# Kernel tuning notes

Hardware: AMD Instinct MI355X
Metric: run time of the kernel (lower is better)

Reference implementation:

```python
import jax, jax.numpy as jnp
import numpy as np
from jax import lax

B, L, D, H, DK, DFF, NL = 8, 128, 512, 8, 64, 2048, 6
T = 3 * L - 1
SC, AC = 14, 73  # state / action channel counts


def _linear(x, w, b):
    return x @ w.T + b


def _ln(x, w, b):
    m = x.mean(-1, keepdims=True)
    v = ((x - m) ** 2).mean(-1, keepdims=True)
    return (x - m) / jnp.sqrt(v + 1e-5) * w + b


def _conv(x, w, b):
    y = lax.conv_general_dilated(x, w, (1, 1), ((1, 1), (1, 1)),
                                 dimension_numbers=('NCHW', 'OIHW', 'NCHW'))
    return y + b[None, :, None, None]


def _convT(x, w, b, s, op):
    # torch ConvTranspose2d(k=3, stride=s, padding=1, output_padding=op)
    wt = jnp.flip(w, (2, 3)).transpose(1, 0, 2, 3)
    y = lax.conv_general_dilated(x, wt, (1, 1), ((1, 1 + op), (1, 1 + op)),
                                 lhs_dilation=(s, s),
                                 dimension_numbers=('NCHW', 'OIHW', 'NCHW'))
    return y + b[None, :, None, None]


def _cnn_enc(x, c1w, c1b, c2w, c2b, c3w, c3b, fcw, fcb, lnw, lnb):
    h = jax.nn.relu(_conv(x, c1w, c1b))
    h = jax.nn.relu(_conv(h, c2w, c2b))
    h = jax.nn.relu(_conv(h, c3w, c3b))
    h = h.reshape(h.shape[0], -1)
    return _ln(_linear(h, fcw, fcb), lnw, lnb)


def _mlp_enc(x, w1, b1, w2, b2, lnw, lnb):
    h = jax.nn.relu(_linear(x, w1, b1))
    return _ln(_linear(h, w2, b2), lnw, lnb)


def _decode(z, fcw, fcb, w1, b1, w2, b2, w3, b3):
    h = jax.nn.relu(_linear(z, fcw, fcb)).reshape(-1, 128, 2, 2)
    h = jax.nn.relu(_convT(h, w1, b1, 2, 1))
    h = jax.nn.relu(_convT(h, w2, b2, 2, 1))
    return _convT(h, w3, b3, 1, 0)


def setup_inputs():
    key = jax.random.key(0)
    cnt = [0]
    def nrm(shape, scale=0.02):
        cnt[0] += 1
        return jax.random.normal(jax.random.fold_in(key, cnt[0]), shape, jnp.float32) * scale
    z = lambda *s: jnp.zeros(s, jnp.float32)
    o = lambda *s: jnp.ones(s, jnp.float32)
    inp = dict(
        states=nrm((B, L, SC, 8, 8), 1.0),
        rtgs=nrm((B, L, 1), 1.0),
        timesteps=jax.random.randint(jax.random.fold_in(key, 9999), (B, L, 1), 0, 512, jnp.int32),
        actions=nrm((B, L - 1, AC, 8, 8), 1.0),
        mask=jnp.tril(jnp.ones((T, T), jnp.int32)),
        se_c1w=nrm((32, SC, 3, 3)), se_c1b=z(32),
        se_c2w=nrm((64, 32, 3, 3)), se_c2b=z(64),
        se_c3w=nrm((64, 64, 3, 3)), se_c3b=z(64),
        se_fcw=nrm((D, 64 * 64)), se_fcb=z(D), se_lnw=o(D), se_lnb=z(D),
        ae_c1w=nrm((32, AC, 3, 3)), ae_c1b=z(32),
        ae_c2w=nrm((64, 32, 3, 3)), ae_c2b=z(64),
        ae_c3w=nrm((64, 64, 3, 3)), ae_c3b=z(64),
        ae_fcw=nrm((D, 64 * 64)), ae_fcb=z(D), ae_lnw=o(D), ae_lnb=z(D),
        rtg_w1=nrm((D, 1)), rtg_b1=z(D), rtg_w2=nrm((D, D)), rtg_b2=z(D), rtg_lnw=o(D), rtg_lnb=z(D),
        ts_w1=nrm((D, 1)), ts_b1=z(D), ts_w2=nrm((D, D)), ts_b2=z(D), ts_lnw=o(D), ts_lnb=z(D),
        ip_w=nrm((D, D)), ip_b=z(D),
        lyr_wq=nrm((NL, D, D)), lyr_bq=z(NL, D),
        lyr_wk=nrm((NL, D, D)), lyr_bk=z(NL, D),
        lyr_wv=nrm((NL, D, D)), lyr_bv=z(NL, D),
        lyr_wo=nrm((NL, D, D)), lyr_bo=z(NL, D),
        lyr_f1w=nrm((NL, DFF, D)), lyr_f1b=z(NL, DFF),
        lyr_f2w=nrm((NL, D, DFF)), lyr_f2b=z(NL, D),
        lyr_l1w=o(NL, D), lyr_l1b=z(NL, D),
        lyr_l2w=o(NL, D), lyr_l2b=z(NL, D),
        ad_fcw=nrm((512, D)), ad_fcb=z(512),
        ad_w1=nrm((128, 64, 3, 3)), ad_b1=z(64),
        ad_w2=nrm((64, 32, 3, 3)), ad_b2=z(32),
        ad_w3=nrm((32, AC, 3, 3)), ad_b3=z(AC),
        sd_fcw=nrm((512, D)), sd_fcb=z(512),
        sd_w1=nrm((128, 64, 3, 3)), sd_b1=z(64),
        sd_w2=nrm((64, 32, 3, 3)), sd_b2=z(32),
        sd_w3=nrm((32, SC, 3, 3)), sd_b3=z(SC),
        rp_w=nrm((1, D)), rp_b=z(1),
    )
    return inp


def reference(states, rtgs, timesteps, actions, mask,
              se_c1w, se_c1b, se_c2w, se_c2b, se_c3w, se_c3b, se_fcw, se_fcb, se_lnw, se_lnb,
              ae_c1w, ae_c1b, ae_c2w, ae_c2b, ae_c3w, ae_c3b, ae_fcw, ae_fcb, ae_lnw, ae_lnb,
              rtg_w1, rtg_b1, rtg_w2, rtg_b2, rtg_lnw, rtg_lnb,
              ts_w1, ts_b1, ts_w2, ts_b2, ts_lnw, ts_lnb,
              ip_w, ip_b,
              lyr_wq, lyr_bq, lyr_wk, lyr_bk, lyr_wv, lyr_bv, lyr_wo, lyr_bo,
              lyr_f1w, lyr_f1b, lyr_f2w, lyr_f2b, lyr_l1w, lyr_l1b, lyr_l2w, lyr_l2b,
              ad_fcw, ad_fcb, ad_w1, ad_b1, ad_w2, ad_b2, ad_w3, ad_b3,
              sd_fcw, sd_fcb, sd_w1, sd_b1, sd_w2, sd_b2, sd_w3, sd_b3,
              rp_w, rp_b):
    b, l = states.shape[:2]
    s_emb = _cnn_enc(states.reshape(b * l, SC, 8, 8), se_c1w, se_c1b, se_c2w, se_c2b,
                     se_c3w, se_c3b, se_fcw, se_fcb, se_lnw, se_lnb).reshape(b, l, D)
    a_emb = _cnn_enc(actions.reshape(b * (l - 1), AC, 8, 8), ae_c1w, ae_c1b, ae_c2w, ae_c2b,
                     ae_c3w, ae_c3b, ae_fcw, ae_fcb, ae_lnw, ae_lnb).reshape(b, l - 1, D)
    r_emb = _mlp_enc(rtgs.reshape(b * l, 1), rtg_w1, rtg_b1, rtg_w2, rtg_b2, rtg_lnw, rtg_lnb).reshape(b, l, D)
    t_emb = _mlp_enc(timesteps.astype(jnp.float32).reshape(b * l, 1), ts_w1, ts_b1, ts_w2, ts_b2, ts_lnw, ts_lnb).reshape(b, l, D)
    # interleave (rtg, state, action) tokens -> length 3L-1
    comb = jnp.zeros((b, 3 * l - 1, D), jnp.float32)
    comb = comb.at[:, 0::3].set(r_emb + t_emb)
    comb = comb.at[:, 1::3].set(s_emb + t_emb)
    comb = comb.at[:, 2::3].set(a_emb + t_emb[:, :-1])
    x = _linear(comb, ip_w, ip_b)  # dropout is identity in eval
    keep = (mask != 0)[None, None]
    scale = 1.0 / float(np.sqrt(DK))

    def block(x, p):
        wq, bq, wk, bk, wv, bv, wo, bo, f1w, f1b, f2w, f2b, l1w, l1b, l2w, l2b = p
        t = x.shape[1]
        q = _linear(x, wq, bq).reshape(b, t, H, DK).transpose(0, 2, 1, 3)
        k = _linear(x, wk, bk).reshape(b, t, H, DK).transpose(0, 2, 1, 3)
        v = _linear(x, wv, bv).reshape(b, t, H, DK).transpose(0, 2, 1, 3)
        sc = jnp.einsum('bhqd,bhkd->bhqk', q, k) * scale
        sc = jnp.where(keep, sc, jnp.float32(-1e9))
        att = jax.nn.softmax(sc, axis=-1)
        o = jnp.einsum('bhqk,bhkd->bhqd', att, v).transpose(0, 2, 1, 3).reshape(b, t, D)
        x = _ln(x + _linear(o, wo, bo), l1w, l1b)
        ff = _linear(jax.nn.relu(_linear(x, f1w, f1b)), f2w, f2b)
        x = _ln(x + ff, l2w, l2b)
        return x, None

    x, _ = lax.scan(block, x, (lyr_wq, lyr_bq, lyr_wk, lyr_bk, lyr_wv, lyr_bv, lyr_wo, lyr_bo,
                               lyr_f1w, lyr_f1b, lyr_f2w, lyr_f2b, lyr_l1w, lyr_l1b, lyr_l2w, lyr_l2b))
    x_state = x[:, ::3]
    x_action = x[:, 1::3]
    x_reward = x[:, 2::3]
    action_preds = _decode(x_action.reshape(-1, D), ad_fcw, ad_fcb, ad_w1, ad_b1, ad_w2, ad_b2, ad_w3, ad_b3).reshape(b, -1, AC, 8, 8)
    state_preds = _decode(x_state.reshape(-1, D), sd_fcw, sd_fcb, sd_w1, sd_b1, sd_w2, sd_b2, sd_w3, sd_b3).reshape(b, -1, SC, 8, 8)
    reward_preds = _linear(x_reward, rp_w, rp_b)
    return action_preds, state_preds, reward_preds
```

## Files before the change

kernel.cpp:

```cpp
#include <hip/hip_runtime.h>


#define TT 383

typedef short      bf16x8 __attribute__((ext_vector_type(8)));
typedef float      f32x4  __attribute__((ext_vector_type(4)));
typedef unsigned short u16x8 __attribute__((ext_vector_type(8)));
typedef unsigned short u16x4 __attribute__((ext_vector_type(4)));

__device__ __forceinline__ unsigned short f2bf(float f)
{
  unsigned u = __float_as_uint(f);
  return (unsigned short)((u + 0x7FFFu + ((u >> 16) & 1u)) >> 16);
}

__global__ __launch_bounds__(256) void cast_bf16_kernel(
    const float* __restrict__ in, unsigned short* __restrict__ out, long n)
{
  long i = ((long)blockIdx.x * 256 + threadIdx.x) * 4;
  if (i >= n) return;
  const float4 v = *(const float4*)(in + i);
  u16x4 o;
  o.x = f2bf(v.x); o.y = f2bf(v.y); o.z = f2bf(v.z); o.w = f2bf(v.w);
  *(u16x4*)(out + i) = o;
}

__global__ __launch_bounds__(256) void merge_qkv_w_kernel(
    const float* __restrict__ wq, const float* __restrict__ wk,
    const float* __restrict__ wv, unsigned short* __restrict__ dst)
{
  long i = ((long)blockIdx.x * 256 + threadIdx.x) * 4;
  if (i >= 6L * 786432) return;
  long l = i / 786432, rem = i % 786432;
  int which = (int)(rem / 262144);
  long o = rem % 262144;
  const float* src = which == 0 ? wq : which == 1 ? wk : wv;
  float4 v = *(const float4*)(src + l * 262144 + o);
  u16x4 w;
  w.x = f2bf(v.x); w.y = f2bf(v.y); w.z = f2bf(v.z); w.w = f2bf(v.w);
  *(u16x4*)(dst + i) = w;
}

__global__ void merge_qkv_b_kernel(const float* __restrict__ bq, const float* __restrict__ bk,
                                   const float* __restrict__ bv, float* __restrict__ dst)
{
  int i = blockIdx.x * 256 + threadIdx.x;
  if (i >= 6 * 1536) return;
  int l = i / 1536, r = i % 1536;
  int which = r >> 9, o = r & 511;
  dst[i] = (which == 0 ? bq : which == 1 ? bk : bv)[l * 512 + o];
}

#define LDAP 72
__global__ __launch_bounds__(256) void gemm_bf16_kernel(
    const unsigned short* __restrict__ A, const unsigned short* __restrict__ B,
    const float* __restrict__ bias, float* __restrict__ C,
    int M, int N, int K, int relu, int obf, int splitK)
{
  __shared__ __align__(16) unsigned short As[128 * LDAP];
  __shared__ __align__(16) unsigned short Bs[128 * LDAP];

  const int tid = threadIdx.x;
  const int lane = tid & 63;
  const int w  = tid >> 6;
  const int wr = w >> 1, wc = w & 1;
  const int m0 = blockIdx.x * 128, n0 = blockIdx.y * 128;
  const int z  = blockIdx.z;

  const int lr = lane & 15;
  const int hi = lane >> 4;

  f32x4 acc[4][4] = {};

  const int r = tid >> 1;
  const int h = tid & 1;

  int mrow = m0 + r; if (mrow >= M) mrow = M - 1;
  const unsigned short* Ap = A + (long)mrow * K + h * 32;
  const unsigned short* Bp = B + (long)(n0 + r) * K + h * 32;
  unsigned short* Asd = As + r * LDAP + h * 32;
  unsigned short* Bsd = Bs + r * LDAP + h * 32;

  const int kLen = K / splitK;
  const int kBeg = z * kLen, kEnd = kBeg + kLen;

  for (int k0 = kBeg; k0 < kEnd; k0 += 64) {
#pragma unroll
    for (int i = 0; i < 4; ++i)
      *(u16x8*)(Asd + i * 8) = *(const u16x8*)(Ap + k0 + i * 8);
#pragma unroll
    for (int i = 0; i < 4; ++i)
      *(u16x8*)(Bsd + i * 8) = *(const u16x8*)(Bp + k0 + i * 8);
    __syncthreads();

#pragma unroll
    for (int kk = 0; kk < 2; ++kk) {
      const int kof = kk * 32 + hi * 8;
      bf16x8 a[4], b[4];
#pragma unroll
      for (int t = 0; t < 4; ++t)
        a[t] = *(const bf16x8*)(As + (wr * 64 + t * 16 + lr) * LDAP + kof);
#pragma unroll
      for (int t = 0; t < 4; ++t)
        b[t] = *(const bf16x8*)(Bs + (wc * 64 + t * 16 + lr) * LDAP + kof);
#pragma unroll
      for (int i = 0; i < 4; ++i)
#pragma unroll
        for (int j = 0; j < 4; ++j)
          acc[i][j] = __builtin_amdgcn_mfma_f32_16x16x32_bf16(a[i], b[j], acc[i][j], 0, 0, 0);
    }
    __syncthreads();
  }

#pragma unroll
  for (int j = 0; j < 4; ++j) {
    const int col = n0 + wc * 64 + j * 16 + lr;
    const float bv = (bias && z == 0) ? bias[col] : 0.f;
#pragma unroll
    for (int i = 0; i < 4; ++i) {
#pragma unroll
      for (int v = 0; v < 4; ++v) {
        int row = m0 + wr * 64 + i * 16 + hi * 4 + v;
        if (row < M) {
          float x = acc[i][j][v] + bv;
          if (splitK > 1) {
            atomicAdd(&C[(long)row * N + col], x);
          } else {
            if (relu) x = fmaxf(x, 0.f);
            if (obf) ((unsigned short*)C)[(long)row * N + col] = f2bf(x);
            else     C[(long)row * N + col] = x;
          }
        }
      }
    }
  }
}

static inline void gemm_bf(hipStream_t st, const unsigned short* A, const unsigned short* B,
                           const float* bias, float* C, int M, int N, int K,
                           int relu = 0, int obf = 0)
{
  dim3 g((M + 127) / 128, N / 128, 1);
  gemm_bf16_kernel<<<g, 256, 0, st>>>(A, B, bias, C, M, N, K, relu, obf, 1);
}

static inline void gemm_sk(hipStream_t st, const unsigned short* A, const unsigned short* B,
                           const float* bias, float* C, int M, int N, int K, int S)
{
  hipMemsetAsync(C, 0, (size_t)M * N * 4, st);
  dim3 g((M + 127) / 128, N / 128, S);
  gemm_bf16_kernel<<<g, 256, 0, st>>>(A, B, bias, C, M, N, K, 0, 0, S);
}

static inline void cast_bf(hipStream_t st, const float* in, unsigned short* out, long n)
{
  cast_bf16_kernel<<<(int)((n / 4 + 255) / 256), 256, 0, st>>>(in, out, n);
}

__global__ __launch_bounds__(256) void attn_kernel(
    const unsigned short* __restrict__ Qkv, unsigned short* __restrict__ Ob)
{
  __shared__ __align__(16) unsigned short Kl[32 * 72];
  __shared__ __align__(16) unsigned short Vt[64 * 40];
  __shared__ __align__(16) unsigned short Pl[4][16 * 40];

  const int tid = threadIdx.x;
  const int lane = tid & 63;
  const int w = tid >> 6;
  const int lr = lane & 15, hi = lane >> 4;
  const int q0 = blockIdx.x * 64;
  const int bh = blockIdx.y;
  const int b = bh >> 3, h = bh & 7;
  const long baseq = (long)b * TT * 1536 + h * 64;
  const long baseo = (long)b * TT * 512 + h * 64;

  const int qrow = q0 + w * 16 + lr;
  const int qr_c = qrow < TT ? qrow : TT - 1;
  bf16x8 qf0 = *(const bf16x8*)(Qkv + baseq + (long)qr_c * 1536 + hi * 8);
  bf16x8 qf1 = *(const bf16x8*)(Qkv + baseq + (long)qr_c * 1536 + 32 + hi * 8);

  float m[4], l[4];
  f32x4 acc[4];
#pragma unroll
  for (int r = 0; r < 4; ++r) { m[r] = -1e30f; l[r] = 0.f; }
#pragma unroll
  for (int c = 0; c < 4; ++c) acc[c] = (f32x4){0.f, 0.f, 0.f, 0.f};

  const int qmax = min(q0 + 63, TT - 1);
  const int nkv = qmax + 1;

  for (int kv0 = 0; kv0 < nkv; kv0 += 32) {
    __syncthreads();
    {
      int e = tid * 8;
      int kv = e >> 6, d = e & 63;
      int skv = kv0 + kv; if (skv >= TT) skv = TT - 1;
      *(u16x8*)(Kl + kv * 72 + d) = *(const u16x8*)(Qkv + baseq + 512 + (long)skv * 1536 + d);
      u16x8 vv = *(const u16x8*)(Qkv + baseq + 1024 + (long)skv * 1536 + d);
#pragma unroll
      for (int j = 0; j < 8; ++j) Vt[(d + j) * 40 + kv] = vv[j];
    }
    __syncthreads();

    f32x4 s[2] = {};
#pragma unroll
    for (int t = 0; t < 2; ++t) {
      bf16x8 k0 = *(const bf16x8*)(Kl + (t * 16 + lr) * 72 + hi * 8);
      bf16x8 k1 = *(const bf16x8*)(Kl + (t * 16 + lr) * 72 + 32 + hi * 8);
      s[t] = __builtin_amdgcn_mfma_f32_16x16x32_bf16(qf0, k0, s[t], 0, 0, 0);
      s[t] = __builtin_amdgcn_mfma_f32_16x16x32_bf16(qf1, k1, s[t], 0, 0, 0);
    }

    const int qq = q0 + w * 16 + hi * 4;
#pragma unroll
    for (int r = 0; r < 4; ++r) {
      float v0 = s[0][r] * 0.125f;
      float v1 = s[1][r] * 0.125f;
      const int qr = qq + r;
      const int kvA = kv0 + lr, kvB = kv0 + 16 + lr;
      if (kvA > qr || kvA >= TT) v0 = -1e30f;
      if (kvB > qr || kvB >= TT) v1 = -1e30f;
      float rm = fmaxf(v0, v1);
      rm = fmaxf(rm, __shfl_xor(rm, 1));
      rm = fmaxf(rm, __shfl_xor(rm, 2));
      rm = fmaxf(rm, __shfl_xor(rm, 4));
      rm = fmaxf(rm, __shfl_xor(rm, 8));
      float mn = fmaxf(m[r], rm);
      float al = expf(m[r] - mn);
      float e0 = expf(v0 - mn);
      float e1 = expf(v1 - mn);
      float rs = e0 + e1;
      rs += __shfl_xor(rs, 1);
      rs += __shfl_xor(rs, 2);
      rs += __shfl_xor(rs, 4);
      rs += __shfl_xor(rs, 8);
      l[r] = l[r] * al + rs;
      m[r] = mn;
#pragma unroll
      for (int c = 0; c < 4; ++c) acc[c][r] *= al;
      Pl[w][(hi * 4 + r) * 40 + lr]      = f2bf(e0);
      Pl[w][(hi * 4 + r) * 40 + 16 + lr] = f2bf(e1);
    }

    bf16x8 pa = *(const bf16x8*)(&Pl[w][lr * 40 + hi * 8]);
#pragma unroll
    for (int c = 0; c < 4; ++c) {
      bf16x8 vf = *(const bf16x8*)(Vt + (c * 16 + lr) * 40 + hi * 8);
      acc[c] = __builtin_amdgcn_mfma_f32_16x16x32_bf16(pa, vf, acc[c], 0, 0, 0);
    }
  }

  float inv[4];
#pragma unroll
  for (int r = 0; r < 4; ++r) inv[r] = 1.0f / l[r];
#pragma unroll
  for (int c = 0; c < 4; ++c) {
#pragma unroll
    for (int r = 0; r < 4; ++r) {
      int qr = q0 + w * 16 + hi * 4 + r;
      if (qr < TT) Ob[baseo + (long)qr * 512 + c * 16 + lr] = f2bf(acc[c][r] * inv[r]);
    }
  }
}

template <int CIN>
__global__ __launch_bounds__(256) void conv3x3_kernel(
    const float* __restrict__ in, const float* __restrict__ w,
    const float* __restrict__ bias, float* __restrict__ out, int Cout)
{
  __shared__ float img[CIN * 100];
  const int n = blockIdx.x;
  const int tid = threadIdx.x;
  for (int i = tid; i < CIN * 100; i += 256) img[i] = 0.f;
  __syncthreads();
  const float* src = in + (long)n * CIN * 64;
  for (int i = tid; i < CIN * 64; i += 256) {
    int ic = i >> 6, p = i & 63;
    img[ic * 100 + ((p >> 3) + 1) * 10 + (p & 7) + 1] = src[i];
  }
  __syncthreads();

  const int y  = tid & 7;
  const int oc = blockIdx.y * 32 + (tid >> 3);
  if (oc >= Cout) return;

  float acc[8];
#pragma unroll
  for (int x = 0; x < 8; ++x) acc[x] = bias[oc];

  const float* wp = w + (long)oc * CIN * 9;
  for (int ic = 0; ic < CIN; ++ic) {
    float wr[9];
#pragma unroll
    for (int q = 0; q < 9; ++q) wr[q] = wp[ic * 9 + q];
    const float* ib = &img[ic * 100 + y * 10];
#pragma unroll
    for (int ky = 0; ky < 3; ++ky) {
      const float* r = ib + ky * 10;
      float c0 = r[0], c1 = r[1];
#pragma unroll
      for (int x = 0; x < 8; ++x) {
        float c2 = r[x + 2];
        acc[x] = fmaf(c0, wr[ky * 3 + 0],
                 fmaf(c1, wr[ky * 3 + 1],
                 fmaf(c2, wr[ky * 3 + 2], acc[x])));
        c0 = c1; c1 = c2;
      }
    }
  }
  float* dst = out + ((long)n * Cout + oc) * 64 + y * 8;
#pragma unroll
  for (int x = 0; x < 8; ++x) dst[x] = fmaxf(acc[x], 0.f);
}

template <int CIN, int IH, int S, int OP, int OH>
__global__ __launch_bounds__(256) void convT_fast_kernel(
    const float* __restrict__ in, const float* __restrict__ w,
    const float* __restrict__ bias, float* __restrict__ out,
    int Cout, int relu, int inRelu)
{
  constexpr int DW = (IH - 1) * S + 3 + OP;
  constexpr int OCPB = 256 / OH;
  __shared__ float img[CIN * DW * DW];

  const int n = blockIdx.x;
  const int tid = threadIdx.x;
  for (int i = tid; i < CIN * DW * DW; i += 256) img[i] = 0.f;
  __syncthreads();
  const float* src = in + (long)n * CIN * IH * IH;
  for (int i = tid; i < CIN * IH * IH; i += 256) {
    int ic = i / (IH * IH), p = i % (IH * IH);
    int iy = p / IH, ix = p % IH;
    float v = src[i];
    if (inRelu) v = fmaxf(v, 0.f);
    img[ic * DW * DW + (1 + iy * S) * DW + (1 + ix * S)] = v;
  }
  __syncthreads();

  const int y  = tid % OH;
  const int oc = blockIdx.y * OCPB + tid / OH;
  if (oc >= Cout) return;

  float acc[OH];
#pragma unroll
  for (int x = 0; x < OH; ++x) acc[x] = bias[oc];

  for (int ic = 0; ic < CIN; ++ic) {
    const float* wp = w + ((long)ic * Cout + oc) * 9;
    float wr[9];
#pragma unroll
    for (int q = 0; q < 9; ++q) wr[q] = wp[8 - q];
    const float* ib = &img[ic * DW * DW + y * DW];
#pragma unroll
    for (int ky = 0; ky < 3; ++ky) {
      const float* r = ib + ky * DW;
      float c0 = r[0], c1 = r[1];
#pragma unroll
      for (int x = 0; x < OH; ++x) {
        float c2 = r[x + 2];
        acc[x] = fmaf(c0, wr[ky * 3 + 0],
                 fmaf(c1, wr[ky * 3 + 1],
                 fmaf(c2, wr[ky * 3 + 2], acc[x])));
        c0 = c1; c1 = c2;
      }
    }
  }
  float* dst = out + ((long)n * Cout + oc) * OH * OH + y * OH;
#pragma unroll
  for (int x = 0; x < OH; ++x) dst[x] = relu ? fmaxf(acc[x], 0.f) : acc[x];
}

__device__ __forceinline__ float blockReduceSum256(float v)
{
  __shared__ float sb[4];
  int lane = threadIdx.x & 63, wid = threadIdx.x >> 6;
#pragma unroll
  for (int o = 32; o; o >>= 1) v += __shfl_down(v, o);
  __syncthreads();
  if (lane == 0) sb[wid] = v;
  __syncthreads();
  return sb[0] + sb[1] + sb[2] + sb[3];
}

__global__ __launch_bounds__(256) void add_ln_kernel(
    const float* __restrict__ a, const float* __restrict__ b,
    const float* __restrict__ w, const float* __restrict__ bb,
    float* __restrict__ out, unsigned short* __restrict__ outbf)
{
  long row = blockIdx.x;
  const float* pa = a + row * 512;
  float x0 = pa[threadIdx.x], x1 = pa[threadIdx.x + 256];
  if (b) {
    const float* pb = b + row * 512;
    x0 += pb[threadIdx.x]; x1 += pb[threadIdx.x + 256];
  }
  float mean = blockReduceSum256(x0 + x1) * (1.f / 512.f);
  float d0 = x0 - mean, d1 = x1 - mean;
  float var = blockReduceSum256(d0 * d0 + d1 * d1) * (1.f / 512.f);
  float inv = 1.0f / sqrtf(var + 1e-5f);
  float v0 = d0 * inv * w[threadIdx.x] + bb[threadIdx.x];
  float v1 = d1 * inv * w[threadIdx.x + 256] + bb[threadIdx.x + 256];
  float* po = out + row * 512;
  po[threadIdx.x]       = v0;
  po[threadIdx.x + 256] = v1;
  if (outbf) {
    outbf[row * 512 + threadIdx.x]       = f2bf(v0);
    outbf[row * 512 + threadIdx.x + 256] = f2bf(v1);
  }
}

__global__ void lin1_relu_kernel(const float* __restrict__ x, const float* __restrict__ w,
                                 const float* __restrict__ b, float* __restrict__ out, long total)
{
  long idx = (long)blockIdx.x * 256 + threadIdx.x;
  if (idx >= total) return;
  int d = idx & 511; long r = idx >> 9;
  out[idx] = fmaxf(fmaf(x[r], w[d], b[d]), 0.f);
}

__global__ void lin1_relu_int_kernel(const int* __restrict__ x, const float* __restrict__ w,
                                     const float* __restrict__ b, float* __restrict__ out, long total)
{
  long idx = (long)blockIdx.x * 256 + threadIdx.x;
  if (idx >= total) return;
  int d = idx & 511; long r = idx >> 9;
  out[idx] = fmaxf(fmaf((float)x[r], w[d], b[d]), 0.f);
}

__global__ void build_comb_kernel(const float* __restrict__ r, const float* __restrict__ s,
                                  const float* __restrict__ a, const float* __restrict__ t,
                                  float* __restrict__ comb)
{
  long idx = (long)blockIdx.x * 256 + threadIdx.x;
  if (idx >= (long)8 * TT * 512) return;
  int d = idx & 511;
  long rr = idx >> 9;
  int tok = (int)(rr % TT);
  int b   = (int)(rr / TT);
  int grp = tok / 3, ph = tok % 3;
  float te = t[((long)b * 128 + grp) * 512 + d];
  float v;
  if (ph == 0)      v = r[((long)b * 128 + grp) * 512 + d] + te;
  else if (ph == 1) v = s[((long)b * 128 + grp) * 512 + d] + te;
  else              v = a[((long)b * 127 + grp) * 512 + d] + te;
  comb[idx] = v;
}

__global__ void gather3_kernel(const float* __restrict__ x, float* __restrict__ out,
                               int offset, int count)
{
  long idx = (long)blockIdx.x * 256 + threadIdx.x;
  long total = (long)8 * count * 512;
  if (idx >= total) return;
  int d = idx & 511;
  long r = idx >> 9;
  int i = (int)(r % count);
  int b = (int)(r / count);
  out[idx] = x[((long)b * TT + offset + 3 * i) * 512 + d];
}

__global__ __launch_bounds__(256) void reward_kernel(const float* __restrict__ x,
                                                     const float* __restrict__ w,
                                                     const float* __restrict__ b,
                                                     float* __restrict__ out, int rows)
{
  int row = blockIdx.x * 4 + (threadIdx.x >> 6);
  int lane = threadIdx.x & 63;
  if (row >= rows) return;
  const float* p = x + (long)row * 512;
  float s = 0.f;
  for (int j = lane; j < 512; j += 64) s = fmaf(p[j], w[j], s);
#pragma unroll
  for (int o = 32; o; o >>= 1) s += __shfl_xor(s, o);
  if (lane == 0) out[row] = s + b[0];
}

extern "C" void kernel_launch(void* const* d_in, const int* in_sizes, int n_in,
                              void* d_out, int out_size, void* d_ws, size_t ws_size,
                              hipStream_t stream)
{
  const float* states  = (const float*)d_in[0];
  const float* rtgs    = (const float*)d_in[1];
  const int*   tsteps  = (const int*)d_in[2];
  const float* actions = (const float*)d_in[3];
  const float* se_c1w = (const float*)d_in[5];  const float* se_c1b = (const float*)d_in[6];
  const float* se_c2w = (const float*)d_in[7];  const float* se_c2b = (const float*)d_in[8];
  const float* se_c3w = (const float*)d_in[9];  const float* se_c3b = (const float*)d_in[10];
  const float* se_fcw = (const float*)d_in[11]; const float* se_fcb = (const float*)d_in[12];
  const float* se_lnw = (const float*)d_in[13]; const float* se_lnb = (const float*)d_in[14];
  const float* ae_c1w = (const float*)d_in[15]; const float* ae_c1b = (const float*)d_in[16];
  const float* ae_c2w = (const float*)d_in[17]; const float* ae_c2b = (const float*)d_in[18];
  const float* ae_c3w = (const float*)d_in[19]; const float* ae_c3b = (const float*)d_in[20];
  const float* ae_fcw = (const float*)d_in[21]; const float* ae_fcb = (const float*)d_in[22];
  const float* ae_lnw = (const float*)d_in[23]; const float* ae_lnb = (const float*)d_in[24];
  const float* rtg_w1 = (const float*)d_in[25]; const float* rtg_b1 = (const float*)d_in[26];
  const float* rtg_w2 = (const float*)d_in[27]; const float* rtg_b2 = (const float*)d_in[28];
  const float* rtg_lnw= (const float*)d_in[29]; const float* rtg_lnb= (const float*)d_in[30];
  const float* ts_w1  = (const float*)d_in[31]; const float* ts_b1  = (const float*)d_in[32];
  const float* ts_w2  = (const float*)d_in[33]; const float* ts_b2  = (const float*)d_in[34];
  const float* ts_lnw = (const float*)d_in[35]; const float* ts_lnb = (const float*)d_in[36];
  const float* ip_w   = (const float*)d_in[37]; const float* ip_b   = (const float*)d_in[38];
  const float* lyr_wq = (const float*)d_in[39]; const float* lyr_bq = (const float*)d_in[40];
  const float* lyr_wk = (const float*)d_in[41]; const float* lyr_bk = (const float*)d_in[42];
  const float* lyr_wv = (const float*)d_in[43]; const float* lyr_bv = (const float*)d_in[44];
  const float* lyr_wo = (const float*)d_in[45]; const float* lyr_bo = (const float*)d_in[46];
  const float* lyr_f1w= (const float*)d_in[47]; const float* lyr_f1b= (const float*)d_in[48];
  const float* lyr_f2w= (const float*)d_in[49]; const float* lyr_f2b= (const float*)d_in[50];
  const float* lyr_l1w= (const float*)d_in[51]; const float* lyr_l1b= (const float*)d_in[52];
  const float* lyr_l2w= (const float*)d_in[53]; const float* lyr_l2b= (const float*)d_in[54];
  const float* ad_fcw = (const float*)d_in[55]; const float* ad_fcb = (const float*)d_in[56];
  const float* ad_w1  = (const float*)d_in[57]; const float* ad_b1  = (const float*)d_in[58];
  const float* ad_w2  = (const float*)d_in[59]; const float* ad_b2  = (const float*)d_in[60];
  const float* ad_w3  = (const float*)d_in[61]; const float* ad_b3  = (const float*)d_in[62];
  const float* sd_fcw = (const float*)d_in[63]; const float* sd_fcb = (const float*)d_in[64];
  const float* sd_w1  = (const float*)d_in[65]; const float* sd_b1  = (const float*)d_in[66];
  const float* sd_w2  = (const float*)d_in[67]; const float* sd_b2  = (const float*)d_in[68];
  const float* sd_w3  = (const float*)d_in[69]; const float* sd_b3  = (const float*)d_in[70];
  const float* rp_w   = (const float*)d_in[71]; const float* rp_b   = (const float*)d_in[72];

  float* ws = (float*)d_ws;
  long off = 0;
  auto alloc = [&](long n) { float* p = ws + off; off += n; return p; };

  float* region = alloc(10485760);
  float* h1 = region;
  float* h2 = region + 2097152;
  float* h3 = region + 6291456;
  float* s_emb = alloc(524288);
  float* a_emb = alloc(520192);
  float* r_emb = alloc(524288);
  float* t_emb = alloc(524288);
  float* etmp  = alloc(524288);
  float* xa = alloc(1568768);
  float* xb = alloc(1568768);
  float* t2 = alloc(1568768);
  float* qkvB = alloc(9216);

  unsigned short* bws = (unsigned short*)(ws + off);
  long boff = 0;
  auto ballo = [&](long n) { unsigned short* p = bws + boff; boff += n; return p; };
  unsigned short* ipW   = ballo(262144);
  unsigned short* wqkvW = ballo(6L * 786432);
  unsigned short* woW   = ballo(6L * 262144);
  unsigned short* f1W   = ballo(6L * 1048576);
  unsigned short* f2W   = ballo(6L * 1048576);
  unsigned short* seW   = ballo(2097152);
  unsigned short* aeW   = ballo(2097152);
  unsigned short* rtgW  = ballo(262144);
  unsigned short* tsW   = ballo(262144);
  unsigned short* adW   = ballo(262144);
  unsigned short* sdW   = ballo(262144);
  unsigned short* qkvbf = ballo(4706304);
  unsigned short* aobf  = ballo(1568768);
  unsigned short* xbfA  = ballo(1568768);
  unsigned short* xbfB  = ballo(1568768);
  unsigned short* ffhbf = ballo(6275072);
  unsigned short* abuf  = ballo(6275072);

  const long BT = (long)8 * TT;

  cast_bf(stream, ip_w,    ipW,  262144);
  merge_qkv_w_kernel<<<(int)((6L * 786432 / 4 + 255) / 256), 256, 0, stream>>>(lyr_wq, lyr_wk, lyr_wv, wqkvW);
  merge_qkv_b_kernel<<<(6 * 1536 + 255) / 256, 256, 0, stream>>>(lyr_bq, lyr_bk, lyr_bv, qkvB);
  cast_bf(stream, lyr_wo,  woW,  6L * 262144);
  cast_bf(stream, lyr_f1w, f1W,  6L * 1048576);
  cast_bf(stream, lyr_f2w, f2W,  6L * 1048576);
  cast_bf(stream, se_fcw,  seW,  2097152);
  cast_bf(stream, ae_fcw,  aeW,  2097152);
  cast_bf(stream, rtg_w2,  rtgW, 262144);
  cast_bf(stream, ts_w2,   tsW,  262144);
  cast_bf(stream, ad_fcw,  adW,  262144);
  cast_bf(stream, sd_fcw,  sdW,  262144);

  conv3x3_kernel<14><<<dim3(1024, 1), 256, 0, stream>>>(states, se_c1w, se_c1b, h1, 32);
  conv3x3_kernel<32><<<dim3(1024, 2), 256, 0, stream>>>(h1, se_c2w, se_c2b, h2, 64);
  conv3x3_kernel<64><<<dim3(1024, 2), 256, 0, stream>>>(h2, se_c3w, se_c3b, h3, 64);
  cast_bf(stream, h3, abuf, 1024L * 4096);
  gemm_sk(stream, abuf, seW, se_fcb, etmp, 1024, 512, 4096, 8);
  add_ln_kernel<<<1024, 256, 0, stream>>>(etmp, nullptr, se_lnw, se_lnb, s_emb, nullptr);

  conv3x3_kernel<73><<<dim3(1016, 1), 256, 0, stream>>>(actions, ae_c1w, ae_c1b, h1, 32);
  conv3x3_kernel<32><<<dim3(1016, 2), 256, 0, stream>>>(h1, ae_c2w, ae_c2b, h2, 64);
  conv3x3_kernel<64><<<dim3(1016, 2), 256, 0, stream>>>(h2, ae_c3w, ae_c3b, h3, 64);
  cast_bf(stream, h3, abuf, 1016L * 4096);
  gemm_sk(stream, abuf, aeW, ae_fcb, etmp, 1016, 512, 4096, 8);
  add_ln_kernel<<<1016, 256, 0, stream>>>(etmp, nullptr, ae_lnw, ae_lnb, a_emb, nullptr);

  lin1_relu_kernel<<<(1024 * 512 + 255) / 256, 256, 0, stream>>>(rtgs, rtg_w1, rtg_b1, t2, 1024 * 512);
  cast_bf(stream, t2, abuf, 1024L * 512);
  gemm_sk(stream, abuf, rtgW, rtg_b2, etmp, 1024, 512, 512, 8);
  add_ln_kernel<<<1024, 256, 0, stream>>>(etmp, nullptr, rtg_lnw, rtg_lnb, r_emb, nullptr);

  lin1_relu_int_kernel<<<(1024 * 512 + 255) / 256, 256, 0, stream>>>(tsteps, ts_w1, ts_b1, t2, 1024 * 512);
  cast_bf(stream, t2, abuf, 1024L * 512);
  gemm_sk(stream, abuf, tsW, ts_b2, etmp, 1024, 512, 512, 8);
  add_ln_kernel<<<1024, 256, 0, stream>>>(etmp, nullptr, ts_lnw, ts_lnb, t_emb, nullptr);

  build_comb_kernel<<<(int)((8L * TT * 512 + 255) / 256), 256, 0, stream>>>(r_emb, s_emb, a_emb, t_emb, xb);
  cast_bf(stream, xb, abuf, BT * 512);
  gemm_sk(stream, abuf, ipW, ip_b, xa, (int)BT, 512, 512, 4);
  cast_bf(stream, xa, xbfA, BT * 512);

  for (int l = 0; l < 6; ++l) {
    const unsigned short* wqkv = wqkvW + (long)l * 786432;
    const float* bqkv = qkvB + (long)l * 1536;
    const unsigned short* wo = woW + (long)l * 262144; const float* bo = lyr_bo + (long)l * 512;
    const unsigned short* f1w = f1W + (long)l * 1048576; const float* f1b = lyr_f1b + (long)l * 2048;
    const unsigned short* f2w = f2W + (long)l * 1048576; const float* f2b = lyr_f2b + (long)l * 512;
    const float* l1w = lyr_l1w + (long)l * 512; const float* l1b = lyr_l1b + (long)l * 512;
    const float* l2w = lyr_l2w + (long)l * 512; const float* l2b = lyr_l2b + (long)l * 512;

    gemm_bf(stream, xbfA, wqkv, bqkv, (float*)qkvbf, (int)BT, 1536, 512, 0, 1);
    attn_kernel<<<dim3(6, 64), 256, 0, stream>>>(qkvbf, aobf);
    gemm_sk(stream, aobf, wo, bo, t2, (int)BT, 512, 512, 4);
    add_ln_kernel<<<(int)BT, 256, 0, stream>>>(xa, t2, l1w, l1b, xb, xbfB);
    gemm_bf(stream, xbfB, f1w, f1b, (float*)ffhbf, (int)BT, 2048, 512, 1, 1);
    gemm_sk(stream, ffhbf, f2w, f2b, t2, (int)BT, 512, 2048, 4);
    add_ln_kernel<<<(int)BT, 256, 0, stream>>>(xb, t2, l2w, l2b, xa, xbfA);
  }

  float* outp = (float*)d_out;
  float* act_out = outp;
  float* st_out  = outp + 4784128;
  float* rw_out  = outp + 5701632;

  float* za  = region;
  float* zfc = region + 524288;
  float* dh1 = region + 1048576;
  float* dh2 = region + 2097152;

  gather3_kernel<<<(1024 * 512 + 255) / 256, 256, 0, stream>>>(xa, za, 1, 128);
  cast_bf(stream, za, abuf, 1024L * 512);
  gemm_sk(stream, abuf, adW, ad_fcb, zfc, 1024, 512, 512, 8);
  convT_fast_kernel<128, 2, 2, 1, 4><<<dim3(1024, 1), 256, 0, stream>>>(zfc, ad_w1, ad_b1, dh1, 64, 1, 1);
  convT_fast_kernel<64, 4, 2, 1, 8><<<dim3(1024, 1), 256, 0, stream>>>(dh1, ad_w2, ad_b2, dh2, 32, 1, 0);
  convT_fast_kernel<32, 8, 1, 0, 8><<<dim3(1024, 3), 256, 0, stream>>>(dh2, ad_w3, ad_b3, act_out, 73, 0, 0);

  gather3_kernel<<<(1024 * 512 + 255) / 256, 256, 0, stream>>>(xa, za, 0, 128);
  cast_bf(stream, za, abuf, 1024L * 512);
  gemm_sk(stream, abuf, sdW, sd_fcb, zfc, 1024, 512, 512, 8);
  convT_fast_kernel<128, 2, 2, 1, 4><<<dim3(1024, 1), 256, 0, stream>>>(zfc, sd_w1, sd_b1, dh1, 64, 1, 1);
  convT_fast_kernel<64, 4, 2, 1, 8><<<dim3(1024, 1), 256, 0, stream>>>(dh1, sd_w2, sd_b2, dh2, 32, 1, 0);
  convT_fast_kernel<32, 8, 1, 0, 8><<<dim3(1024, 1), 256, 0, stream>>>(dh2, sd_w3, sd_b3, st_out, 14, 0, 0);

  gather3_kernel<<<(1016 * 512 + 255) / 256, 256, 0, stream>>>(xa, za, 2, 127);
  reward_kernel<<<(1016 + 3) / 4, 256, 0, stream>>>(za, rp_w, rp_b, rw_out, 1016);
}
```

Baseline: 2.058 ms.

## Replace scalar encoder convolutions with bf16 MFMA implicit-GEMM in NHWC padded layout

The fp32 scalar 3x3 conv kernels in the state and action encoders are replaced by an implicit-GEMM kernel on bf16 MFMA. It works on a zero-padded, channel-last (NHWC-style) bf16 layout with weights repacked per tap, and the FC weight is permuted to match the new flatten order. The lin1, relu and comb kernels now write bf16 directly, which removes separate cast passes. The FF2 split-K factor goes from 4 to 8. This adds memsets, repack kernels and bf16 rounding of the conv activations.

After: 1.997 ms. 2.9% less time.

```diff
diff --git a/kernel.cpp b/kernel.cpp
--- a/kernel.cpp
+++ b/kernel.cpp
@@ -49,6 +49,129 @@
   int l = i / 1536, r = i % 1536;
   int which = r >> 9, o = r & 511;
   dst[i] = (which == 0 ? bq : which == 1 ? bk : bv)[l * 512 + o];
+}
+
+__global__ void cast_perm_fc_kernel(const float* __restrict__ in, unsigned short* __restrict__ out)
+{
+  long i = (long)blockIdx.x * 256 + threadIdx.x;
+  if (i >= 512L * 4096) return;
+  int o = (int)(i >> 12);
+  int r = (int)(i & 4095);
+  int p = r >> 6, c = r & 63;
+  out[i] = f2bf(in[((long)o << 12) + c * 64 + p]);
+}
+
+__global__ void wtap_kernel(const float* __restrict__ w, unsigned short* __restrict__ dst,
+                            int CIN, int CINP, int NOUT)
+{
+  int i = blockIdx.x * 256 + threadIdx.x;
+  int total = 9 * NOUT * CINP;
+  if (i >= total) return;
+  int t = i / (NOUT * CINP);
+  int rem = i % (NOUT * CINP);
+  int oc = rem / CINP, icp = rem % CINP;
+  float v = icp < CIN ? w[(((long)oc * CIN + icp) * 3 + t / 3) * 3 + t % 3] : 0.f;
+  dst[i] = f2bf(v);
+}
+
+__global__ void pad_repack_kernel(const float* __restrict__ in, unsigned short* __restrict__ dst,
+                                  int N, int CIN, int CINP)
+{
+  long i = (long)blockIdx.x * 256 + threadIdx.x;
+  long total = (long)N * 64 * CINP;
+  if (i >= total) return;
+  int chp = (int)(i % CINP);
+  long r = i / CINP;
+  int p = (int)(r & 63);
+  int n = (int)(r >> 6);
+  float v = chp < CIN ? in[((long)n * CIN + chp) * 64 + p] : 0.f;
+  int y = p >> 3, x = p & 7;
+  dst[((long)n * 100 + (y + 1) * 10 + (x + 1)) * CINP + chp] = f2bf(v);
+}
+
+template <int CINP, int NOUT, int PADOUT>
+__global__ __launch_bounds__(256) void conv_mfma_kernel(
+    const unsigned short* __restrict__ src, const unsigned short* __restrict__ wt,
+    const float* __restrict__ bias, unsigned short* __restrict__ dst)
+{
+  constexpr int PITCH = CINP + 8;
+  constexpr int WN = (NOUT == 64) ? 2 : 1;
+  constexpr int ROWS = 128 / (4 / WN);
+  constexpr int AI = ROWS / 16;
+  constexpr int KC = CINP / 32;
+
+  __shared__ __align__(16) unsigned short img[200 * PITCH];
+  __shared__ __align__(16) unsigned short Bs[NOUT * PITCH];
+
+  const int tid = threadIdx.x;
+  const int lane = tid & 63;
+  const int w = tid >> 6;
+  const int wr = w / WN, wc = w % WN;
+  const int lr = lane & 15, hi = lane >> 4;
+  const int n0 = blockIdx.x * 2;
+
+  {
+    const unsigned short* g = src + (long)n0 * 100 * CINP;
+    for (int e = tid * 8; e < 200 * CINP; e += 2048) {
+      int row = e / CINP, k = e % CINP;
+      *(u16x8*)(img + row * PITCH + k) = *(const u16x8*)(g + e);
+    }
+  }
+
+  f32x4 acc[AI][2];
+#pragma unroll
+  for (int i = 0; i < AI; ++i)
+#pragma unroll
+    for (int j = 0; j < 2; ++j) acc[i][j] = (f32x4){0.f, 0.f, 0.f, 0.f};
+
+#pragma unroll
+  for (int t = 0; t < 9; ++t) {
+    const int ky = t / 3, kx = t % 3;
+    for (int e = tid * 8; e < NOUT * CINP; e += 2048) {
+      int oc = e / CINP, k = e % CINP;
+      *(u16x8*)(Bs + oc * PITCH + k) = *(const u16x8*)(wt + t * NOUT * CINP + e);
+    }
+    __syncthreads();
+#pragma unroll
+    for (int kc = 0; kc < KC; ++kc) {
+      bf16x8 a[AI], b[2];
+#pragma unroll
+      for (int i = 0; i < AI; ++i) {
+        int row = wr * ROWS + i * 16 + lr;
+        int lrow = (row >> 6) * 100 + (((row >> 3) & 7) + ky) * 10 + (row & 7) + kx;
+        a[i] = *(const bf16x8*)(img + lrow * PITCH + kc * 32 + hi * 8);
+      }
+#pragma unroll
+      for (int j = 0; j < 2; ++j)
+        b[j] = *(const bf16x8*)(Bs + (wc * 32 + j * 16 + lr) * PITCH + kc * 32 + hi * 8);
+#pragma unroll
+      for (int i = 0; i < AI; ++i)
+#pragma unroll
+        for (int j = 0; j < 2; ++j)
+          acc[i][j] = __builtin_amdgcn_mfma_f32_16x16x32_bf16(a[i], b[j], acc[i][j], 0, 0, 0);
+    }
+    __syncthreads();
+  }
+
+#pragma unroll
+  for (int j = 0; j < 2; ++j) {
+    const int col = wc * 32 + j * 16 + lr;
+    const float bv = bias[col];
+#pragma unroll
+    for (int i = 0; i < AI; ++i) {
+#pragma unroll
+      for (int v = 0; v < 4; ++v) {
+        int row = wr * ROWS + i * 16 + hi * 4 + v;
+        unsigned short o = f2bf(fmaxf(acc[i][j][v] + bv, 0.f));
+        if (PADOUT) {
+          int nl = row >> 6, y = (row >> 3) & 7, xx = row & 7;
+          dst[((long)(n0 + nl) * 100 + (y + 1) * 10 + (xx + 1)) * NOUT + col] = o;
+        } else {
+          dst[((long)blockIdx.x * 128 + row) * NOUT + col] = o;
+        }
+      }
+    }
+  }
 }
 
 #define LDAP 72
@@ -263,56 +386,6 @@
   }
 }
 
-template <int CIN>
-__global__ __launch_bounds__(256) void conv3x3_kernel(
-    const float* __restrict__ in, const float* __restrict__ w,
-    const float* __restrict__ bias, float* __restrict__ out, int Cout)
-{
-  __shared__ float img[CIN * 100];
-  const int n = blockIdx.x;
-  const int tid = threadIdx.x;
-  for (int i = tid; i < CIN * 100; i += 256) img[i] = 0.f;
-  __syncthreads();
-  const float* src = in + (long)n * CIN * 64;
-  for (int i = tid; i < CIN * 64; i += 256) {
-    int ic = i >> 6, p = i & 63;
-    img[ic * 100 + ((p >> 3) + 1) * 10 + (p & 7) + 1] = src[i];
-  }
-  __syncthreads();
-
-  const int y  = tid & 7;
-  const int oc = blockIdx.y * 32 + (tid >> 3);
-  if (oc >= Cout) return;
-
-  float acc[8];
-#pragma unroll
-  for (int x = 0; x < 8; ++x) acc[x] = bias[oc];
-
-  const float* wp = w + (long)oc * CIN * 9;
-  for (int ic = 0; ic < CIN; ++ic) {
-    float wr[9];
-#pragma unroll
-    for (int q = 0; q < 9; ++q) wr[q] = wp[ic * 9 + q];
-    const float* ib = &img[ic * 100 + y * 10];
-#pragma unroll
-    for (int ky = 0; ky < 3; ++ky) {
-      const float* r = ib + ky * 10;
-      float c0 = r[0], c1 = r[1];
-#pragma unroll
-      for (int x = 0; x < 8; ++x) {
-        float c2 = r[x + 2];
-        acc[x] = fmaf(c0, wr[ky * 3 + 0],
-                 fmaf(c1, wr[ky * 3 + 1],
-                 fmaf(c2, wr[ky * 3 + 2], acc[x])));
-        c0 = c1; c1 = c2;
-      }
-    }
-  }
-  float* dst = out + ((long)n * Cout + oc) * 64 + y * 8;
-#pragma unroll
-  for (int x = 0; x < 8; ++x) dst[x] = fmaxf(acc[x], 0.f);
-}
-
 template <int CIN, int IH, int S, int OP, int OH>
 __global__ __launch_bounds__(256) void convT_fast_kernel(
     const float* __restrict__ in, const float* __restrict__ w,
@@ -409,27 +482,29 @@
   }
 }
 
-__global__ void lin1_relu_kernel(const float* __restrict__ x, const float* __restrict__ w,
-                                 const float* __restrict__ b, float* __restrict__ out, long total)
+__global__ void lin1_relu_bf_kernel(const float* __restrict__ x, const float* __restrict__ w,
+                                    const float* __restrict__ b, unsigned short* __restrict__ out,
+                                    long total)
 {
   long idx = (long)blockIdx.x * 256 + threadIdx.x;
   if (idx >= total) return;
   int d = idx & 511; long r = idx >> 9;
-  out[idx] = fmaxf(fmaf(x[r], w[d], b[d]), 0.f);
-}
-
-__global__ void lin1_relu_int_kernel(const int* __restrict__ x, const float* __restrict__ w,
-                                     const float* __restrict__ b, float* __restrict__ out, long total)
+  out[idx] = f2bf(fmaxf(fmaf(x[r], w[d], b[d]), 0.f));
+}
+
+__global__ void lin1_relu_int_bf_kernel(const int* __restrict__ x, const float* __restrict__ w,
+                                        const float* __restrict__ b, unsigned short* __restrict__ out,
+                                        long total)
 {
   long idx = (long)blockIdx.x * 256 + threadIdx.x;
   if (idx >= total) return;
   int d = idx & 511; long r = idx >> 9;
-  out[idx] = fmaxf(fmaf((float)x[r], w[d], b[d]), 0.f);
-}
-
-__global__ void build_comb_kernel(const float* __restrict__ r, const float* __restrict__ s,
-                                  const float* __restrict__ a, const float* __restrict__ t,
-                                  float* __restrict__ comb)
+  out[idx] = f2bf(fmaxf(fmaf((float)x[r], w[d], b[d]), 0.f));
+}
+
+__global__ void build_comb_bf_kernel(const float* __restrict__ r, const float* __restrict__ s,
+                                     const float* __restrict__ a, const float* __restrict__ t,
+                                     unsigned short* __restrict__ comb)
 {
   long idx = (long)blockIdx.x * 256 + threadIdx.x;
   if (idx >= (long)8 * TT * 512) return;
@@ -443,7 +518,7 @@
   if (ph == 0)      v = r[((long)b * 128 + grp) * 512 + d] + te;
   else if (ph == 1) v = s[((long)b * 128 + grp) * 512 + d] + te;
   else              v = a[((long)b * 127 + grp) * 512 + d] + te;
-  comb[idx] = v;
+  comb[idx] = f2bf(v);
 }
 
 __global__ void gather3_kernel(const float* __restrict__ x, float* __restrict__ out,
@@ -523,9 +598,6 @@
   auto alloc = [&](long n) { float* p = ws + off; off += n; return p; };
 
   float* region = alloc(10485760);
-  float* h1 = region;
-  float* h2 = region + 2097152;
-  float* h3 = region + 6291456;
   float* s_emb = alloc(524288);
   float* a_emb = alloc(520192);
   float* r_emb = alloc(524288);
@@ -544,12 +616,18 @@
   unsigned short* woW   = ballo(6L * 262144);
   unsigned short* f1W   = ballo(6L * 1048576);
   unsigned short* f2W   = ballo(6L * 1048576);
-  unsigned short* seW   = ballo(2097152);
-  unsigned short* aeW   = ballo(2097152);
+  unsigned short* seWp  = ballo(2097152);
+  unsigned short* aeWp  = ballo(2097152);
   unsigned short* rtgW  = ballo(262144);
   unsigned short* tsW   = ballo(262144);
   unsigned short* adW   = ballo(262144);
   unsigned short* sdW   = ballo(262144);
+  unsigned short* wtSE1 = ballo(9216);
+  unsigned short* wtSE2 = ballo(18432);
+  unsigned short* wtSE3 = ballo(36864);
+  unsigned short* wtAE1 = ballo(27648);
+  unsigned short* wtAE2 = ballo(18432);
+  unsigned short* wtAE3 = ballo(36864);
   unsigned short* qkvbf = ballo(4706304);
   unsigned short* aobf  = ballo(1568768);
   unsigned short* xbfA  = ballo(1568768);
@@ -557,6 +635,11 @@
   unsigned short* ffhbf = ballo(6275072);
   unsigned short* abuf  = ballo(6275072);
 
+  unsigned short* P1  = (unsigned short*)region;
+  unsigned short* Po1 = P1 + 9830400;
+  unsigned short* Po2 = Po1 + 3276800;
+  unsigned short* c3o = ffhbf;
+
   const long BT = (long)8 * TT;
 
   cast_bf(stream, ip_w,    ipW,  262144);
@@ -565,39 +648,48 @@
   cast_bf(stream, lyr_wo,  woW,  6L * 262144);
   cast_bf(stream, lyr_f1w, f1W,  6L * 1048576);
   cast_bf(stream, lyr_f2w, f2W,  6L * 1048576);
-  cast_bf(stream, se_fcw,  seW,  2097152);
-  cast_bf(stream, ae_fcw,  aeW,  2097152);
+  cast_perm_fc_kernel<<<(int)((512L * 4096 + 255) / 256), 256, 0, stream>>>(se_fcw, seWp);
+  cast_perm_fc_kernel<<<(int)((512L * 4096 + 255) / 256), 256, 0, stream>>>(ae_fcw, aeWp);
   cast_bf(stream, rtg_w2,  rtgW, 262144);
   cast_bf(stream, ts_w2,   tsW,  262144);
   cast_bf(stream, ad_fcw,  adW,  262144);
   cast_bf(stream, sd_fcw,  sdW,  262144);
-
-  conv3x3_kernel<14><<<dim3(1024, 1), 256, 0, stream>>>(states, se_c1w, se_c1b, h1, 32);
-  conv3x3_kernel<32><<<dim3(1024, 2), 256, 0, stream>>>(h1, se_c2w, se_c2b, h2, 64);
-  conv3x3_kernel<64><<<dim3(1024, 2), 256, 0, stream>>>(h2, se_c3w, se_c3b, h3, 64);
-  cast_bf(stream, h3, abuf, 1024L * 4096);
-  gemm_sk(stream, abuf, seW, se_fcb, etmp, 1024, 512, 4096, 8);
+  wtap_kernel<<<(9 * 32 * 32 + 255) / 256, 256, 0, stream>>>(se_c1w, wtSE1, 14, 32, 32);
+  wtap_kernel<<<(9 * 64 * 32 + 255) / 256, 256, 0, stream>>>(se_c2w, wtSE2, 32, 32, 64);
+  wtap_kernel<<<(9 * 64 * 64 + 255) / 256, 256, 0, stream>>>(se_c3w, wtSE3, 64, 64, 64);
+  wtap_kernel<<<(9 * 32 * 96 + 255) / 256, 256, 0, stream>>>(ae_c1w, wtAE1, 73, 96, 32);
+  wtap_kernel<<<(9 * 64 * 32 + 255) / 256, 256, 0, stream>>>(ae_c2w, wtAE2, 32, 32, 64);
+  wtap_kernel<<<(9 * 64 * 64 + 255) / 256, 256, 0, stream>>>(ae_c3w, wtAE3, 64, 64, 64);
+
+  hipMemsetAsync(P1, 0, 1024L * 100 * 32 * 2, stream);
+  pad_repack_kernel<<<(int)((1024L * 64 * 32 + 255) / 256), 256, 0, stream>>>(states, P1, 1024, 14, 32);
+  hipMemsetAsync(Po1, 0, 1024L * 100 * 32 * 2, stream);
+  conv_mfma_kernel<32, 32, 1><<<512, 256, 0, stream>>>(P1, wtSE1, se_c1b, Po1);
+  hipMemsetAsync(Po2, 0, 1024L * 100 * 64 * 2, stream);
+  conv_mfma_kernel<32, 64, 1><<<512, 256, 0, stream>>>(Po1, wtSE2, se_c2b, Po2);
+  conv_mfma_kernel<64, 64, 0><<<512, 256, 0, stream>>>(Po2, wtSE3, se_c3b, c3o);
+  gemm_sk(stream, c3o, seWp, se_fcb, etmp, 1024, 512, 4096, 8);
   add_ln_kernel<<<1024, 256, 0, stream>>>(etmp, nullptr, se_lnw, se_lnb, s_emb, nullptr);
 
-  conv3x3_kernel<73><<<dim3(1016, 1), 256, 0, stream>>>(actions, ae_c1w, ae_c1b, h1, 32);
-  conv3x3_kernel<32><<<dim3(1016, 2), 256, 0, stream>>>(h1, ae_c2w, ae_c2b, h2, 64);
-  conv3x3_kernel<64><<<dim3(1016, 2), 256, 0, stream>>>(h2, ae_c3w, ae_c3b, h3, 64);
-  cast_bf(stream, h3, abuf, 1016L * 4096);
-  gemm_sk(stream, abuf, aeW, ae_fcb, etmp, 1016, 512, 4096, 8);
+  hipMemsetAsync(P1, 0, 1016L * 100 * 96 * 2, stream);
+  pad_repack_kernel<<<(int)((1016L * 64 * 96 + 255) / 256), 256, 0, stream>>>(actions, P1, 1016, 73, 96);
+  hipMemsetAsync(Po1, 0, 1016L * 100 * 32 * 2, stream);
+  conv_mfma_kernel<96, 32, 1><<<508, 256, 0, stream>>>(P1, wtAE1, ae_c1b, Po1);
+  hipMemsetAsync(Po2, 0, 1016L * 100 * 64 * 2, stream);
+  conv_mfma_kernel<32, 64, 1><<<508, 256, 0, stream>>>(Po1, wtAE2, ae_c2b, Po2);
+  conv_mfma_kernel<64, 64, 0><<<508, 256, 0, stream>>>(Po2, wtAE3, ae_c3b, c3o);
+  gemm_sk(stream, c3o, aeWp, ae_fcb, etmp, 1016, 512, 4096, 8);
   add_ln_kernel<<<1016, 256, 0, stream>>>(etmp, nullptr, ae_lnw, ae_lnb, a_emb, nullptr);
 
-  lin1_relu_kernel<<<(1024 * 512 + 255) / 256, 256, 0, stream>>>(rtgs, rtg_w1, rtg_b1, t2, 1024 * 512);
-  cast_bf(stream, t2, abuf, 1024L * 512);
+  lin1_relu_bf_kernel<<<(1024 * 512 + 255) / 256, 256, 0, stream>>>(rtgs, rtg_w1, rtg_b1, abuf, 1024 * 512);
   gemm_sk(stream, abuf, rtgW, rtg_b2, etmp, 1024, 512, 512, 8);
   add_ln_kernel<<<1024, 256, 0, stream>>>(etmp, nullptr, rtg_lnw, rtg_lnb, r_emb, nullptr);
 
-  lin1_relu_int_kernel<<<(1024 * 512 + 255) / 256, 256, 0, stream>>>(tsteps, ts_w1, ts_b1, t2, 1024 * 512);
-  cast_bf(stream, t2, abuf, 1024L * 512);
+  lin1_relu_int_bf_kernel<<<(1024 * 512 + 255) / 256, 256, 0, stream>>>(tsteps, ts_w1, ts_b1, abuf, 1024 * 512);
   gemm_sk(stream, abuf, tsW, ts_b2, etmp, 1024, 512, 512, 8);
   add_ln_kernel<<<1024, 256, 0, stream>>>(etmp, nullptr, ts_lnw, ts_lnb, t_emb, nullptr);
 
-  build_comb_kernel<<<(int)((8L * TT * 512 + 255) / 256), 256, 0, stream>>>(r_emb, s_emb, a_emb, t_emb, xb);
-  cast_bf(stream, xb, abuf, BT * 512);
+  build_comb_bf_kernel<<<(int)((8L * TT * 512 + 255) / 256), 256, 0, stream>>>(r_emb, s_emb, a_emb, t_emb, abuf);
   gemm_sk(stream, abuf, ipW, ip_b, xa, (int)BT, 512, 512, 4);
   cast_bf(stream, xa, xbfA, BT * 512);
 
@@ -615,7 +707,7 @@
     gemm_sk(stream, aobf, wo, bo, t2, (int)BT, 512, 512, 4);
     add_ln_kernel<<<(int)BT, 256, 0, stream>>>(xa, t2, l1w, l1b, xb, xbfB);
     gemm_bf(stream, xbfB, f1w, f1b, (float*)ffhbf, (int)BT, 2048, 512, 1, 1);
-    gemm_sk(stream, ffhbf, f2w, f2b, t2, (int)BT, 512, 2048, 4);
+    gemm_sk(stream, ffhbf, f2w, f2b, t2, (int)BT, 512, 2048, 8);
     add_ln_kernel<<<(int)BT, 256, 0, stream>>>(xb, t2, l2w, l2b, xa, xbfA);
   }
 
```
